# Kernel optimization log

Measured on AMD Instinct MI355X. Metric: run time of the kernel, lower is better.

Reference implementation:

```python
import jax, jax.numpy as jnp
import numpy as np

B, NX, NC, C, H = 4, 1024, 2048, 1024, 16
DH = C // H            # head_dim = 64
SCALE = DH ** -0.5


def setup_inputs() -> dict:
    key = jax.random.key(0)
    ks = jax.random.split(key, 6)
    # sorted unique token indices to update per batch (== positions where update_mask==1)
    rng = np.random.default_rng(0)
    idx = np.stack([np.sort(rng.permutation(NC)[:NX]) for _ in range(B)]).astype(np.int32)
    return {
        "x": jax.random.normal(ks[0], (B, NX, C), jnp.float32),
        "update_idx": jnp.asarray(idx),                              # (B, NX) int32
        "cache_k": jax.random.normal(ks[1], (B, H, NC, DH), jnp.float32),
        "cache_v": jax.random.normal(ks[2], (B, H, NC, DH), jnp.float32),
        "w_qkv": jax.random.normal(ks[3], (3 * C, C), jnp.float32) * 0.02,
        "b_qkv": jnp.zeros((3 * C,), jnp.float32),
        "w_proj": jax.random.normal(ks[4], (C, C), jnp.float32) * 0.02,
        "b_proj": jnp.zeros((C,), jnp.float32),
    }


def reference(x, update_idx, cache_k, cache_v, w_qkv, b_qkv, w_proj, b_proj):
    Bq, N, Cq = x.shape
    # QKV projection: (B, N, 3C) -> (3, B, H, N, Dh) layout as in torch permute(2,0,3,1,4)
    qkv = (x @ w_qkv.T + b_qkv).reshape(Bq, N, 3, H, DH)
    q = qkv[:, :, 0].transpose(0, 2, 1, 3)  # (B, H, N, Dh)
    k = qkv[:, :, 1].transpose(0, 2, 1, 3)
    v = qkv[:, :, 2].transpose(0, 2, 1, 3)
    # masked_scatter_ of k/v into cache at the masked (updated) token slots.
    # Indices are sorted, so row-order masked_scatter == indexed scatter.
    scat = jax.vmap(lambda cache, idx, src: cache.at[:, idx, :].set(src))
    k_full = scat(cache_k, update_idx, k)    # (B, H, NC, Dh)
    v_full = scat(cache_v, update_idx, v)
    # plain attention: q scaled, full softmax over cache length
    attn = jax.nn.softmax(jnp.einsum('bhqd,bhkd->bhqk', q * SCALE, k_full), axis=-1)
    out = jnp.einsum('bhqk,bhkd->bhqd', attn, v_full)  # (B, H, N, Dh)
    out = out.transpose(0, 2, 1, 3).reshape(Bq, N, Cq)
    return out @ w_proj.T + b_proj
```

## Files before the change

kernel.cpp:

```cpp
#include <hip/hip_runtime.h>
#include <hip/hip_bf16.h>

#define B_   4
#define NX_  1024
#define NC_  2048
#define C_   1024
#define H_   16
#define DH_  64

typedef __attribute__((ext_vector_type(8))) __bf16 bf16x8;
typedef __attribute__((ext_vector_type(4))) float  f32x4;

static __device__ __forceinline__ unsigned short f2bf(float f) {
    unsigned int u = __float_as_uint(f);
    u += 0x7fffu + ((u >> 16) & 1u);
    return (unsigned short)(u >> 16);
}

static __device__ __forceinline__ unsigned int pk2(float lo, float hi) {
    unsigned int a = __float_as_uint(lo) + 0x8000u;
    unsigned int b = __float_as_uint(hi) + 0x8000u;
    return __builtin_amdgcn_perm(b, a, 0x07060302);
}

static __device__ __forceinline__ bf16x8 ldfrag(const unsigned short* p) {
    union { uint4 u; bf16x8 b; } cv;
    cv.u = *reinterpret_cast<const uint4*>(p);
    return cv.b;
}

__global__ __launch_bounds__(256) void cvt_all_kernel(
    const float* __restrict__ x,  const float* __restrict__ wq,
    const float* __restrict__ wp, const float* __restrict__ ck,
    const float* __restrict__ cv_,
    unsigned short* __restrict__ xbf,  unsigned short* __restrict__ wqbf,
    unsigned short* __restrict__ wpbf, unsigned short* __restrict__ kfb,
    unsigned short* __restrict__ vt) {
    int blk = blockIdx.x;
    if (blk < 16384) {
        const float* src; unsigned short* dst; int i;
        if (blk < 4096)      { src = x;  dst = xbf;  i = blk; }
        else if (blk < 7168) { src = wq; dst = wqbf; i = blk - 4096; }
        else if (blk < 8192) { src = wp; dst = wpbf; i = blk - 7168; }
        else                 { src = ck; dst = kfb;  i = blk - 8192; }
        int idx = i * 256 + threadIdx.x;
        float4 f = reinterpret_cast<const float4*>(src)[idx];
        ushort4 o;
        o.x = f2bf(f.x); o.y = f2bf(f.y); o.z = f2bf(f.z); o.w = f2bf(f.w);
        reinterpret_cast<ushort4*>(dst)[idx] = o;
    } else {
        int i   = blk - 16384;
        int t   = threadIdx.x;
        int bh  = i >> 6;
        int kg  = i & 63;
        int d   = t & 63;
        int kci = t >> 6;
        int kc  = kg * 4 + kci;
        const float* src = cv_ + ((size_t)bh * NC_ + (size_t)kc * 8) * DH_ + d;
        union { uint4 u; unsigned short s[8]; } o;
#pragma unroll
        for (int j = 0; j < 8; j++) o.s[j] = f2bf(src[(size_t)j * DH_]);
        *reinterpret_cast<uint4*>(vt + ((size_t)bh * DH_ + d) * NC_ + (size_t)kc * 8) = o.u;
    }
}

#define LSTR 40

__global__ __launch_bounds__(256, 3) void qkv_gemm_kernel(
    const unsigned short* __restrict__ xbf,
    const unsigned short* __restrict__ wbf,
    const float* __restrict__ bias,
    const int* __restrict__ uidx,
    unsigned short* __restrict__ qb,
    unsigned short* __restrict__ kf,
    unsigned short* __restrict__ vt)
{
    __shared__ unsigned short As[128 * LSTR], Bs[128 * LSTR];
    int bn = blockIdx.x, bm = blockIdx.y;
    int w = threadIdx.x >> 6, l = threadIdx.x & 63;
    int quad = l >> 4, col = l & 15;
    int wr = w >> 1, wc = w & 1;
    int srow = w * 32 + (l >> 2), schk = (l & 3) * 8;

    const unsigned short* Ap = xbf + (size_t)(bm * 128 + srow) * C_ + schk;
    const unsigned short* Bp = wbf + (size_t)(bn * 128 + srow) * C_ + schk;
    unsigned short* Aw = As + srow * LSTR + schk;
    unsigned short* Bw = Bs + srow * LSTR + schk;

    f32x4 acc[4][4];
#pragma unroll
    for (int a = 0; a < 4; a++)
#pragma unroll
        for (int b = 0; b < 4; b++) acc[a][b] = (f32x4){0.f, 0.f, 0.f, 0.f};

    uint4 ar0, ar1, br0, br1;
#define LDREG(kk_)                                                       \
    {   int kk = (kk_) * 32;                                             \
        ar0 = *reinterpret_cast<const uint4*>(Ap + kk);                  \
        ar1 = *reinterpret_cast<const uint4*>(Ap + 16 * C_ + kk);        \
        br0 = *reinterpret_cast<const uint4*>(Bp + kk);                  \
        br1 = *reinterpret_cast<const uint4*>(Bp + 16 * C_ + kk);        \
    }
#define WRTILE()                                                         \
    {   *reinterpret_cast<uint4*>(Aw)             = ar0;                 \
        *reinterpret_cast<uint4*>(Aw + 16 * LSTR) = ar1;                 \
        *reinterpret_cast<uint4*>(Bw)             = br0;                 \
        *reinterpret_cast<uint4*>(Bw + 16 * LSTR) = br1;                 \
    }

    LDREG(0);
    WRTILE();
    LDREG(1);
    __syncthreads();
#pragma unroll 1
    for (int it = 0; it < 32; it++) {
        bf16x8 af[4], bfr[4];
#pragma unroll
        for (int t = 0; t < 4; t++) af[t]  = ldfrag(&As[(wr * 64 + t * 16 + col) * LSTR + quad * 8]);
#pragma unroll
        for (int t = 0; t < 4; t++) bfr[t] = ldfrag(&Bs[(wc * 64 + t * 16 + col) * LSTR + quad * 8]);
#pragma unroll
        for (int mt = 0; mt < 4; mt++)
#pragma unroll
            for (int nt = 0; nt < 4; nt++)
                acc[mt][nt] = __builtin_amdgcn_mfma_f32_16x16x32_bf16(af[mt], bfr[nt], acc[mt][nt], 0, 0, 0);
        if (it < 31) {
            __syncthreads();
            WRTILE();
            LDREG(it + 2 < 31 ? it + 2 : 31);
            __syncthreads();
        }
    }
#undef LDREG
#undef WRTILE

    int part = bn >> 3;
    float bv[4]; int nl[4];
#pragma unroll
    for (int nt = 0; nt < 4; nt++) {
        int n = bn * 128 + wc * 64 + nt * 16 + col;
        bv[nt] = bias[n];
        nl[nt] = n & 1023;
    }
    const float QS = 0.18033688011112042f;
#pragma unroll
    for (int mt = 0; mt < 4; mt++)
#pragma unroll
        for (int r = 0; r < 4; r++) {
            int m = bm * 128 + wr * 64 + mt * 16 + quad * 4 + r;
            int b = m >> 10, i = m & 1023;
            int j = (part == 0) ? 0 : uidx[(b << 10) + i];
#pragma unroll
            for (int nt = 0; nt < 4; nt++) {
                int h = nl[nt] >> 6, d = nl[nt] & 63;
                float v = acc[mt][nt][r] + bv[nt];
                if (part == 0)
                    qb[((size_t)(b * H_ + h) * NX_ + i) * DH_ + d] = f2bf(v * QS);
                else if (part == 1)
                    kf[((size_t)(b * H_ + h) * NC_ + j) * DH_ + d] = f2bf(v);
                else
                    vt[((size_t)(b * H_ + h) * DH_ + d) * NC_ + j] = f2bf(v);
            }
        }
}

#define PST 40
__global__ __launch_bounds__(256, 4) void attn_kernel(
    const unsigned short* __restrict__ qb,
    const unsigned short* __restrict__ kf,
    const unsigned short* __restrict__ vt,
    unsigned short* __restrict__ ao)
{
    __shared__ unsigned short Klo[64 * LSTR], Khi[64 * LSTR];
    __shared__ unsigned short V0s[64 * LSTR], V1s[64 * LSTR];
    __shared__ unsigned short Psh[4][16 * PST];
    int id = blockIdx.x;
    int qt = (id >> 3) & 15;
    int bh = ((id >> 7) << 3) | (id & 7);
    int wave = threadIdx.x >> 6, lane = threadIdx.x & 63;
    int quad = lane >> 4, col = lane & 15;
    int srow = wave * 16 + (lane >> 2), schk = (lane & 3) * 8;

    const unsigned short* qrow = qb + ((size_t)bh * NX_ + qt * 64 + wave * 16 + col) * DH_;
    bf16x8 qf0 = ldfrag(qrow + quad * 8);
    bf16x8 qf1 = ldfrag(qrow + 32 + quad * 8);

    const unsigned short* Kp = kf + ((size_t)bh * NC_ + srow) * DH_ + schk;
    const unsigned short* Vp = vt + ((size_t)bh * DH_ + srow) * NC_ + schk;
    unsigned short* Kwl = Klo + srow * LSTR + schk;
    unsigned short* Kwh = Khi + srow * LSTR + schk;
    unsigned short* Vw0 = V0s + srow * LSTR + schk;
    unsigned short* Vw1 = V1s + srow * LSTR + schk;
    unsigned short* Pw = &Psh[wave][0];

    f32x4 o[4];
#pragma unroll
    for (int t = 0; t < 4; t++) o[t] = (f32x4){0.f, 0.f, 0.f, 0.f};
    float l_i = 0.f;

    uint4 kr0, kr1, vr0, vr1;
#define LDREG(kb_)                                                        \
    {   kr0 = *reinterpret_cast<const uint4*>(Kp + (size_t)(kb_) * 64 * DH_);      \
        kr1 = *reinterpret_cast<const uint4*>(Kp + (size_t)(kb_) * 64 * DH_ + 32); \
        vr0 = *reinterpret_cast<const uint4*>(Vp + (kb_) * 64);           \
        vr1 = *reinterpret_cast<const uint4*>(Vp + (kb_) * 64 + 32);      \
    }
#define WRTILE()                                                          \
    {   *reinterpret_cast<uint4*>(Kwl) = kr0;                             \
        *reinterpret_cast<uint4*>(Kwh) = kr1;                             \
        *reinterpret_cast<uint4*>(Vw0) = vr0;                             \
        *reinterpret_cast<uint4*>(Vw1) = vr1;                             \
    }

    LDREG(0);
    WRTILE();
    LDREG(1);
    __syncthreads();

#pragma unroll 1
    for (int kb = 0; kb < 32; kb++) {
#pragma unroll
        for (int ks = 0; ks < 2; ks++) {
            f32x4 s0 = (f32x4){0.f, 0.f, 0.f, 0.f};
            f32x4 s1 = (f32x4){0.f, 0.f, 0.f, 0.f};
            {
                bf16x8 a0 = ldfrag(&Klo[(ks * 32 +      col) * LSTR + quad * 8]);
                bf16x8 b0 = ldfrag(&Khi[(ks * 32 +      col) * LSTR + quad * 8]);
                bf16x8 a1 = ldfrag(&Klo[(ks * 32 + 16 + col) * LSTR + quad * 8]);
                bf16x8 b1 = ldfrag(&Khi[(ks * 32 + 16 + col) * LSTR + quad * 8]);
                s0 = __builtin_amdgcn_mfma_f32_16x16x32_bf16(a0, qf0, s0, 0, 0, 0);
                s0 = __builtin_amdgcn_mfma_f32_16x16x32_bf16(b0, qf1, s0, 0, 0, 0);
                s1 = __builtin_amdgcn_mfma_f32_16x16x32_bf16(a1, qf0, s1, 0, 0, 0);
                s1 = __builtin_amdgcn_mfma_f32_16x16x32_bf16(b1, qf1, s1, 0, 0, 0);
            }
            const unsigned short* Vs = (ks == 0) ? V0s : V1s;
            bf16x8 vfr[4];
#pragma unroll
            for (int t = 0; t < 4; t++) vfr[t] = ldfrag(&Vs[(t * 16 + col) * LSTR + quad * 8]);
            {
                float p0 = exp2f(s0[0]), p1 = exp2f(s0[1]), p2 = exp2f(s0[2]), p3 = exp2f(s0[3]);
                float p4 = exp2f(s1[0]), p5 = exp2f(s1[1]), p6 = exp2f(s1[2]), p7 = exp2f(s1[3]);
                l_i += ((p0 + p1) + (p2 + p3)) + ((p4 + p5) + (p6 + p7));
                uint2 w0; w0.x = pk2(p0, p1); w0.y = pk2(p2, p3);
                uint2 w1; w1.x = pk2(p4, p5); w1.y = pk2(p6, p7);
                *reinterpret_cast<uint2*>(&Pw[col * PST +      quad * 4]) = w0;
                *reinterpret_cast<uint2*>(&Pw[col * PST + 16 + quad * 4]) = w1;
            }
            asm volatile("" ::: "memory");
            {
                bf16x8 pf = ldfrag(&Pw[col * PST + quad * 8]);
#pragma unroll
                for (int t = 0; t < 4; t++)
                    o[t] = __builtin_amdgcn_mfma_f32_16x16x32_bf16(vfr[t], pf, o[t], 0, 0, 0);
            }
            asm volatile("" ::: "memory");
        }
        if (kb < 31) {
            __syncthreads();
            WRTILE();
            LDREG(kb + 2 < 31 ? kb + 2 : 31);
            __syncthreads();
        }
    }
#undef LDREG
#undef WRTILE

    l_i += __shfl_xor(l_i, 16, 64);
    l_i += __shfl_xor(l_i, 32, 64);
    float inv = 1.f / l_i;

    int b = bh >> 4, h = bh & 15;
    int q = qt * 64 + wave * 16 + col;
    unsigned short* orow = ao + ((size_t)b * NX_ + q) * C_ + h * 64;
#pragma unroll
    for (int t = 0; t < 4; t++) {
        uint2 ov;
        ov.x = pk2(o[t][0] * inv, o[t][1] * inv);
        ov.y = pk2(o[t][2] * inv, o[t][3] * inv);
        *reinterpret_cast<uint2*>(&orow[t * 16 + quad * 4]) = ov;
    }
}

__global__ __launch_bounds__(256, 3) void proj_gemm_kernel(
    const unsigned short* __restrict__ abf,
    const unsigned short* __restrict__ wbf,
    const float* __restrict__ bias,
    float* __restrict__ out)
{
    __shared__ unsigned short As[128 * LSTR], Bs[64 * LSTR];
    int bn = blockIdx.x, bm = blockIdx.y;
    int w = threadIdx.x >> 6, l = threadIdx.x & 63;
    int quad = l >> 4, col = l & 15;
    int sarow = w * 32 + (l >> 2), sbrow = w * 16 + (l >> 2), schk = (l & 3) * 8;

    const unsigned short* Ap = abf + (size_t)(bm * 128 + sarow) * C_ + schk;
    const unsigned short* Bp = wbf + (size_t)(bn * 64 + sbrow) * C_ + schk;
    unsigned short* Aw = As + sarow * LSTR + schk;
    unsigned short* Bw = Bs + sbrow * LSTR + schk;

    f32x4 acc[2][4];
#pragma unroll
    for (int a = 0; a < 2; a++)
#pragma unroll
        for (int b = 0; b < 4; b++) acc[a][b] = (f32x4){0.f, 0.f, 0.f, 0.f};

    uint4 ar0, ar1, br0;
#define LDREG(kk_)                                                       \
    {   int kk = (kk_) * 32;                                             \
        ar0 = *reinterpret_cast<const uint4*>(Ap + kk);                  \
        ar1 = *reinterpret_cast<const uint4*>(Ap + 16 * C_ + kk);        \
        br0 = *reinterpret_cast<const uint4*>(Bp + kk);                  \
    }
#define WRTILE()                                                         \
    {   *reinterpret_cast<uint4*>(Aw)             = ar0;                 \
        *reinterpret_cast<uint4*>(Aw + 16 * LSTR) = ar1;                 \
        *reinterpret_cast<uint4*>(Bw)             = br0;                 \
    }

    LDREG(0);
    WRTILE();
    LDREG(1);
    __syncthreads();
#pragma unroll 1
    for (int it = 0; it < 32; it++) {
        bf16x8 af[2], bfr[4];
#pragma unroll
        for (int t = 0; t < 2; t++) af[t]  = ldfrag(&As[(w * 32 + t * 16 + col) * LSTR + quad * 8]);
#pragma unroll
        for (int t = 0; t < 4; t++) bfr[t] = ldfrag(&Bs[(t * 16 + col) * LSTR + quad * 8]);
#pragma unroll
        for (int mt = 0; mt < 2; mt++)
#pragma unroll
            for (int nt = 0; nt < 4; nt++)
                acc[mt][nt] = __builtin_amdgcn_mfma_f32_16x16x32_bf16(af[mt], bfr[nt], acc[mt][nt], 0, 0, 0);
        if (it < 31) {
            __syncthreads();
            WRTILE();
            LDREG(it + 2 < 31 ? it + 2 : 31);
            __syncthreads();
        }
    }
#undef LDREG
#undef WRTILE

    float bv[4];
#pragma unroll
    for (int nt = 0; nt < 4; nt++) bv[nt] = bias[bn * 64 + nt * 16 + col];
#pragma unroll
    for (int mt = 0; mt < 2; mt++)
#pragma unroll
        for (int r = 0; r < 4; r++) {
            int m = bm * 128 + w * 32 + mt * 16 + quad * 4 + r;
#pragma unroll
            for (int nt = 0; nt < 4; nt++) {
                int n = bn * 64 + nt * 16 + col;
                out[(size_t)m * C_ + n] = acc[mt][nt][r] + bv[nt];
            }
        }
}

extern "C" void kernel_launch(void* const* d_in, const int* in_sizes, int n_in,
                              void* d_out, int out_size, void* d_ws, size_t ws_size,
                              hipStream_t stream) {
    const float* x      = (const float*)d_in[0];
    const int*   uidx   = (const int*)  d_in[1];
    const float* cachek = (const float*)d_in[2];
    const float* cachev = (const float*)d_in[3];
    const float* wqkv   = (const float*)d_in[4];
    const float* bqkv   = (const float*)d_in[5];
    const float* wproj  = (const float*)d_in[6];
    const float* bproj  = (const float*)d_in[7];
    float* out = (float*)d_out;

    char* ws = (char*)d_ws;
    unsigned short* xbf  = (unsigned short*)(ws);
    unsigned short* wqbf = (unsigned short*)(ws + (8ull  << 20));
    unsigned short* wpbf = (unsigned short*)(ws + (14ull << 20));
    unsigned short* qb   = (unsigned short*)(ws + (16ull << 20));
    unsigned short* kfb  = (unsigned short*)(ws + (24ull << 20));
    unsigned short* vtb  = (unsigned short*)(ws + (40ull << 20));
    unsigned short* aob  = (unsigned short*)(ws + (56ull << 20));

    cvt_all_kernel<<<20480, 256, 0, stream>>>(x, wqkv, wproj, cachek, cachev,
                                              xbf, wqbf, wpbf, kfb, vtb);
    qkv_gemm_kernel <<<dim3(24, 32), 256, 0, stream>>>(xbf, wqbf, bqkv, uidx, qb, kfb, vtb);
    attn_kernel     <<<1024, 256, 0, stream>>>(qb, kfb, vtb, aob);
    proj_gemm_kernel<<<dim3(16, 32), 256, 0, stream>>>(aob, wpbf, bproj, out);
}
```

Measured before the change: 272.2 us.

## Split attention waves over query and key halves; coalesce V-transpose scatter via LDS

The attention kernel now assigns each wave 32 queries and half of each 64-key block, instead of 16 queries over the whole block. Each K and V fragment read from LDS therefore feeds two MFMAs. The two key-half partial outputs and row sums are combined through shared memory at the end. Separately, the V part of the QKV GEMM epilogue stages its tile in LDS and writes transposed V rows so that lanes store consecutive cache positions, replacing scattered 2-byte stores. The changes add register pressure, an extra LDS reduction with barriers, and serialized rounds in the epilogue.

```diff
diff --git a/kernel.cpp b/kernel.cpp
--- a/kernel.cpp
+++ b/kernel.cpp
@@ -76,6 +76,7 @@
     unsigned short* __restrict__ vt)
 {
     __shared__ unsigned short As[128 * LSTR], Bs[128 * LSTR];
+    __shared__ int jtab[128];
     int bn = blockIdx.x, bm = blockIdx.y;
     int w = threadIdx.x >> 6, l = threadIdx.x & 63;
     int quad = l >> 4, col = l & 15;
@@ -135,33 +136,60 @@
 #undef WRTILE
 
     int part = bn >> 3;
-    float bv[4]; int nl[4];
-#pragma unroll
-    for (int nt = 0; nt < 4; nt++) {
-        int n = bn * 128 + wc * 64 + nt * 16 + col;
-        bv[nt] = bias[n];
-        nl[nt] = n & 1023;
-    }
-    const float QS = 0.18033688011112042f;
-#pragma unroll
-    for (int mt = 0; mt < 4; mt++)
-#pragma unroll
-        for (int r = 0; r < 4; r++) {
-            int m = bm * 128 + wr * 64 + mt * 16 + quad * 4 + r;
-            int b = m >> 10, i = m & 1023;
-            int j = (part == 0) ? 0 : uidx[(b << 10) + i];
-#pragma unroll
-            for (int nt = 0; nt < 4; nt++) {
-                int h = nl[nt] >> 6, d = nl[nt] & 63;
-                float v = acc[mt][nt][r] + bv[nt];
-                if (part == 0)
-                    qb[((size_t)(b * H_ + h) * NX_ + i) * DH_ + d] = f2bf(v * QS);
-                else if (part == 1)
-                    kf[((size_t)(b * H_ + h) * NC_ + j) * DH_ + d] = f2bf(v);
-                else
-                    vt[((size_t)(b * H_ + h) * DH_ + d) * NC_ + j] = f2bf(v);
-            }
-        }
+    float bv[4];
+#pragma unroll
+    for (int nt = 0; nt < 4; nt++) bv[nt] = bias[bn * 128 + wc * 64 + nt * 16 + col];
+
+    if (part <= 1) {
+        int nl[4];
+#pragma unroll
+        for (int nt = 0; nt < 4; nt++) nl[nt] = (bn * 128 + wc * 64 + nt * 16 + col) & 1023;
+        const float QS = 0.18033688011112042f;
+#pragma unroll
+        for (int mt = 0; mt < 4; mt++)
+#pragma unroll
+            for (int r = 0; r < 4; r++) {
+                int m = bm * 128 + wr * 64 + mt * 16 + quad * 4 + r;
+                int b = m >> 10, i = m & 1023;
+                int j = (part == 0) ? 0 : uidx[m];
+#pragma unroll
+                for (int nt = 0; nt < 4; nt++) {
+                    int h = nl[nt] >> 6, d = nl[nt] & 63;
+                    float v = acc[mt][nt][r] + bv[nt];
+                    if (part == 0)
+                        qb[((size_t)(b * H_ + h) * NX_ + i) * DH_ + d] = f2bf(v * QS);
+                    else
+                        kf[((size_t)(b * H_ + h) * NC_ + j) * DH_ + d] = f2bf(v);
+                }
+            }
+    } else {
+        if (threadIdx.x < 128) jtab[threadIdx.x] = uidx[bm * 128 + threadIdx.x];
+        __syncthreads();
+        int h = ((bn * 128 + wc * 64) & 1023) >> 6;
+        int b = (bm * 128) >> 10;
+        unsigned short* T = (wc == 0) ? As : Bs;
+        int jv = jtab[wr * 64 + l];
+        unsigned short* vb2 = vt + ((size_t)(b * H_ + h) * 64) * NC_ + jv;
+#pragma unroll 1
+        for (int round = 0; round < 2; round++) {
+            if (wr == round) {
+#pragma unroll
+                for (int nt = 0; nt < 4; nt++)
+#pragma unroll
+                    for (int mt = 0; mt < 4; mt++) {
+                        uint2 pk;
+                        pk.x = pk2(acc[mt][nt][0] + bv[nt], acc[mt][nt][1] + bv[nt]);
+                        pk.y = pk2(acc[mt][nt][2] + bv[nt], acc[mt][nt][3] + bv[nt]);
+                        *reinterpret_cast<uint2*>(&T[(nt * 16 + col) * 72 + mt * 16 + quad * 4]) = pk;
+                    }
+                asm volatile("s_waitcnt lgkmcnt(0)" ::: "memory");
+#pragma unroll 1
+                for (int d = 0; d < 64; d++)
+                    vb2[(size_t)d * NC_] = T[d * 72 + l];
+            }
+            __syncthreads();
+        }
+    }
 }
 
 #define PST 40
@@ -171,19 +199,30 @@
     const unsigned short* __restrict__ vt,
     unsigned short* __restrict__ ao)
 {
-    __shared__ unsigned short Klo[64 * LSTR], Khi[64 * LSTR];
-    __shared__ unsigned short V0s[64 * LSTR], V1s[64 * LSTR];
-    __shared__ unsigned short Psh[4][16 * PST];
+    __shared__ __align__(16) char smem[20480 + 10240];
+    unsigned short* Klo = (unsigned short*)smem;
+    unsigned short* Khi = Klo + 64 * LSTR;
+    unsigned short* V0s = Khi + 64 * LSTR;
+    unsigned short* V1s = V0s + 64 * LSTR;
+    unsigned short* Psh = (unsigned short*)(smem + 20480);
+    float* Om = (float*)smem;
+    float* Lm = Om + 2 * 32 * 64;
+
     int id = blockIdx.x;
     int qt = (id >> 3) & 15;
     int bh = ((id >> 7) << 3) | (id & 7);
     int wave = threadIdx.x >> 6, lane = threadIdx.x & 63;
     int quad = lane >> 4, col = lane & 15;
+    int qh = wave & 1;
+    int kh = wave >> 1;
     int srow = wave * 16 + (lane >> 2), schk = (lane & 3) * 8;
 
-    const unsigned short* qrow = qb + ((size_t)bh * NX_ + qt * 64 + wave * 16 + col) * DH_;
-    bf16x8 qf0 = ldfrag(qrow + quad * 8);
-    bf16x8 qf1 = ldfrag(qrow + 32 + quad * 8);
+    const unsigned short* qrow0 = qb + ((size_t)bh * NX_ + qt * 64 + qh * 32 + col) * DH_;
+    bf16x8 qfA[2], qfB[2];
+    qfA[0] = ldfrag(qrow0 + quad * 8);
+    qfB[0] = ldfrag(qrow0 + 32 + quad * 8);
+    qfA[1] = ldfrag(qrow0 + 16 * DH_ + quad * 8);
+    qfB[1] = ldfrag(qrow0 + 16 * DH_ + 32 + quad * 8);
 
     const unsigned short* Kp = kf + ((size_t)bh * NC_ + srow) * DH_ + schk;
     const unsigned short* Vp = vt + ((size_t)bh * DH_ + srow) * NC_ + schk;
@@ -191,12 +230,17 @@
     unsigned short* Kwh = Khi + srow * LSTR + schk;
     unsigned short* Vw0 = V0s + srow * LSTR + schk;
     unsigned short* Vw1 = V1s + srow * LSTR + schk;
-    unsigned short* Pw = &Psh[wave][0];
-
-    f32x4 o[4];
-#pragma unroll
-    for (int t = 0; t < 4; t++) o[t] = (f32x4){0.f, 0.f, 0.f, 0.f};
-    float l_i = 0.f;
+    unsigned short* Pw0 = Psh + (wave * 2 + 0) * 16 * PST;
+    unsigned short* Pw1 = Psh + (wave * 2 + 1) * 16 * PST;
+    const unsigned short* Vs = kh ? V1s : V0s;
+    int kq = kh * 32;
+
+    f32x4 o[4][2];
+#pragma unroll
+    for (int m = 0; m < 4; m++)
+#pragma unroll
+        for (int n = 0; n < 2; n++) o[m][n] = (f32x4){0.f, 0.f, 0.f, 0.f};
+    float l_i[2] = {0.f, 0.f};
 
     uint4 kr0, kr1, vr0, vr1;
 #define LDREG(kb_)                                                        \
@@ -219,42 +263,48 @@
 
 #pragma unroll 1
     for (int kb = 0; kb < 32; kb++) {
-#pragma unroll
-        for (int ks = 0; ks < 2; ks++) {
-            f32x4 s0 = (f32x4){0.f, 0.f, 0.f, 0.f};
-            f32x4 s1 = (f32x4){0.f, 0.f, 0.f, 0.f};
-            {
-                bf16x8 a0 = ldfrag(&Klo[(ks * 32 +      col) * LSTR + quad * 8]);
-                bf16x8 b0 = ldfrag(&Khi[(ks * 32 +      col) * LSTR + quad * 8]);
-                bf16x8 a1 = ldfrag(&Klo[(ks * 32 + 16 + col) * LSTR + quad * 8]);
-                bf16x8 b1 = ldfrag(&Khi[(ks * 32 + 16 + col) * LSTR + quad * 8]);
-                s0 = __builtin_amdgcn_mfma_f32_16x16x32_bf16(a0, qf0, s0, 0, 0, 0);
-                s0 = __builtin_amdgcn_mfma_f32_16x16x32_bf16(b0, qf1, s0, 0, 0, 0);
-                s1 = __builtin_amdgcn_mfma_f32_16x16x32_bf16(a1, qf0, s1, 0, 0, 0);
-                s1 = __builtin_amdgcn_mfma_f32_16x16x32_bf16(b1, qf1, s1, 0, 0, 0);
-            }
-            const unsigned short* Vs = (ks == 0) ? V0s : V1s;
-            bf16x8 vfr[4];
-#pragma unroll
-            for (int t = 0; t < 4; t++) vfr[t] = ldfrag(&Vs[(t * 16 + col) * LSTR + quad * 8]);
-            {
-                float p0 = exp2f(s0[0]), p1 = exp2f(s0[1]), p2 = exp2f(s0[2]), p3 = exp2f(s0[3]);
-                float p4 = exp2f(s1[0]), p5 = exp2f(s1[1]), p6 = exp2f(s1[2]), p7 = exp2f(s1[3]);
-                l_i += ((p0 + p1) + (p2 + p3)) + ((p4 + p5) + (p6 + p7));
-                uint2 w0; w0.x = pk2(p0, p1); w0.y = pk2(p2, p3);
-                uint2 w1; w1.x = pk2(p4, p5); w1.y = pk2(p6, p7);
-                *reinterpret_cast<uint2*>(&Pw[col * PST +      quad * 4]) = w0;
-                *reinterpret_cast<uint2*>(&Pw[col * PST + 16 + quad * 4]) = w1;
-            }
-            asm volatile("" ::: "memory");
-            {
-                bf16x8 pf = ldfrag(&Pw[col * PST + quad * 8]);
-#pragma unroll
-                for (int t = 0; t < 4; t++)
-                    o[t] = __builtin_amdgcn_mfma_f32_16x16x32_bf16(vfr[t], pf, o[t], 0, 0, 0);
-            }
-            asm volatile("" ::: "memory");
-        }
+        f32x4 s[2][2];
+#pragma unroll
+        for (int mt = 0; mt < 2; mt++)
+#pragma unroll
+            for (int nt = 0; nt < 2; nt++) s[mt][nt] = (f32x4){0.f, 0.f, 0.f, 0.f};
+#pragma unroll
+        for (int mt = 0; mt < 2; mt++) {
+            bf16x8 ka = ldfrag(&Klo[(kq + mt * 16 + col) * LSTR + quad * 8]);
+            bf16x8 kb_ = ldfrag(&Khi[(kq + mt * 16 + col) * LSTR + quad * 8]);
+#pragma unroll
+            for (int nt = 0; nt < 2; nt++) {
+                s[mt][nt] = __builtin_amdgcn_mfma_f32_16x16x32_bf16(ka,  qfA[nt], s[mt][nt], 0, 0, 0);
+                s[mt][nt] = __builtin_amdgcn_mfma_f32_16x16x32_bf16(kb_, qfB[nt], s[mt][nt], 0, 0, 0);
+            }
+        }
+        bf16x8 vfr[4];
+#pragma unroll
+        for (int t = 0; t < 4; t++) vfr[t] = ldfrag(&Vs[(t * 16 + col) * LSTR + quad * 8]);
+#pragma unroll
+        for (int nt = 0; nt < 2; nt++) {
+            unsigned short* Pw = nt ? Pw1 : Pw0;
+            float p0 = exp2f(s[0][nt][0]), p1 = exp2f(s[0][nt][1]);
+            float p2 = exp2f(s[0][nt][2]), p3 = exp2f(s[0][nt][3]);
+            float p4 = exp2f(s[1][nt][0]), p5 = exp2f(s[1][nt][1]);
+            float p6 = exp2f(s[1][nt][2]), p7 = exp2f(s[1][nt][3]);
+            l_i[nt] += ((p0 + p1) + (p2 + p3)) + ((p4 + p5) + (p6 + p7));
+            uint2 w0; w0.x = pk2(p0, p1); w0.y = pk2(p2, p3);
+            uint2 w1; w1.x = pk2(p4, p5); w1.y = pk2(p6, p7);
+            *reinterpret_cast<uint2*>(&Pw[col * PST +      quad * 4]) = w0;
+            *reinterpret_cast<uint2*>(&Pw[col * PST + 16 + quad * 4]) = w1;
+        }
+        asm volatile("" ::: "memory");
+        {
+            bf16x8 pf0 = ldfrag(&Pw0[col * PST + quad * 8]);
+            bf16x8 pf1 = ldfrag(&Pw1[col * PST + quad * 8]);
+#pragma unroll
+            for (int mt = 0; mt < 4; mt++) {
+                o[mt][0] = __builtin_amdgcn_mfma_f32_16x16x32_bf16(vfr[mt], pf0, o[mt][0], 0, 0, 0);
+                o[mt][1] = __builtin_amdgcn_mfma_f32_16x16x32_bf16(vfr[mt], pf1, o[mt][1], 0, 0, 0);
+            }
+        }
+        asm volatile("" ::: "memory");
         if (kb < 31) {
             __syncthreads();
             WRTILE();
@@ -265,19 +315,49 @@
 #undef LDREG
 #undef WRTILE
 
-    l_i += __shfl_xor(l_i, 16, 64);
-    l_i += __shfl_xor(l_i, 32, 64);
-    float inv = 1.f / l_i;
-
-    int b = bh >> 4, h = bh & 15;
-    int q = qt * 64 + wave * 16 + col;
-    unsigned short* orow = ao + ((size_t)b * NX_ + q) * C_ + h * 64;
-#pragma unroll
-    for (int t = 0; t < 4; t++) {
-        uint2 ov;
-        ov.x = pk2(o[t][0] * inv, o[t][1] * inv);
-        ov.y = pk2(o[t][2] * inv, o[t][3] * inv);
-        *reinterpret_cast<uint2*>(&orow[t * 16 + quad * 4]) = ov;
+#pragma unroll
+    for (int nt = 0; nt < 2; nt++) {
+        l_i[nt] += __shfl_xor(l_i[nt], 16, 64);
+        l_i[nt] += __shfl_xor(l_i[nt], 32, 64);
+    }
+
+    __syncthreads();
+    if (kh == 1) {
+#pragma unroll
+        for (int mt = 0; mt < 4; mt++)
+#pragma unroll
+            for (int nt = 0; nt < 2; nt++)
+#pragma unroll
+                for (int r = 0; r < 4; r++)
+                    Om[(qh * 32 + (mt * 2 + nt) * 4 + r) * 64 + lane] = o[mt][nt][r];
+        if (quad == 0) {
+            Lm[(qh * 2 + 0) * 16 + col] = l_i[0];
+            Lm[(qh * 2 + 1) * 16 + col] = l_i[1];
+        }
+    }
+    __syncthreads();
+    if (kh == 0) {
+        float inv[2];
+#pragma unroll
+        for (int nt = 0; nt < 2; nt++)
+            inv[nt] = 1.f / (l_i[nt] + Lm[(qh * 2 + nt) * 16 + col]);
+        int b = bh >> 4, h = bh & 15;
+#pragma unroll
+        for (int mt = 0; mt < 4; mt++)
+#pragma unroll
+            for (int nt = 0; nt < 2; nt++) {
+                int base = (qh * 32 + (mt * 2 + nt) * 4) * 64 + lane;
+                float v0 = (o[mt][nt][0] + Om[base])       * inv[nt];
+                float v1 = (o[mt][nt][1] + Om[base + 64])  * inv[nt];
+                float v2 = (o[mt][nt][2] + Om[base + 128]) * inv[nt];
+                float v3 = (o[mt][nt][3] + Om[base + 192]) * inv[nt];
+                int q = qt * 64 + qh * 32 + nt * 16 + col;
+                uint2 ov;
+                ov.x = pk2(v0, v1);
+                ov.y = pk2(v2, v3);
+                *reinterpret_cast<uint2*>(ao + ((size_t)b * NX_ + q) * C_ +
+                                          h * 64 + mt * 16 + quad * 4) = ov;
+            }
     }
 }
 
```

After: 262.7 us. 1.04x faster.
